# Kernel tuning notes

Hardware: AMD Instinct MI355X
Metric: run time of the kernel (lower is better)

The kernel has to match this reference:

```python
import jax, jax.numpy as jnp
import numpy as np

TEMP = 5.0          # temperature_attn
BN_EPS = 1e-5
L2_EPS = 1e-8

def _conv2d(x, w):
    # x: [N,C,H,W], w: [O,C,3,3], SAME padding, stride 1
    return jax.lax.conv_general_dilated(x, w, (1, 1), 'SAME',
                                        dimension_numbers=('NCHW', 'OIHW', 'NCHW'))

def _conv_over_base(x, w):
    # separable 4D conv piece: 2D conv over the (Hb,Wb) pair of the 6D tensor
    BN, C, Hm, Wm, Hb, Wb = x.shape
    O = w.shape[0]
    y = _conv2d(x.transpose(0, 2, 3, 1, 4, 5).reshape(BN * Hm * Wm, C, Hb, Wb), w)
    return y.reshape(BN, Hm, Wm, O, Hb, Wb).transpose(0, 3, 1, 2, 4, 5)

def _conv_over_mem(x, w):
    # separable 4D conv piece: 2D conv over the (Hm,Wm) pair of the 6D tensor
    BN, C, Hm, Wm, Hb, Wb = x.shape
    O = w.shape[0]
    y = _conv2d(x.transpose(0, 4, 5, 1, 2, 3).reshape(BN * Hb * Wb, C, Hm, Wm), w)
    return y.reshape(BN, Hb, Wb, O, Hm, Wm).transpose(0, 3, 4, 5, 1, 2)

def _l2norm(x, axis):
    n = jnp.sqrt(jnp.sum(x * x, axis=axis, keepdims=True))
    return x / jnp.maximum(n, L2_EPS)

def _gaussian_normalize(x, axis):
    m = jnp.mean(x, axis=axis, keepdims=True)
    v = jnp.var(x, axis=axis, ddof=1, keepdims=True)  # torch.var is unbiased
    return (x - m) / jnp.sqrt(v + BN_EPS)

def setup_inputs() -> dict:
    key = jax.random.key(0)
    ks = jax.random.split(key, 10)
    B, N, C, H = 8, 64, 512, 10
    R, HID, NCLS = 64, 16, 100
    f32 = jnp.float32
    return {
        'feat_b': jax.random.normal(ks[0], (B, C, H, H), f32),
        'feat_m': jax.random.normal(ks[1], (N, C, H, H), f32),
        'w1x1':  jax.random.normal(ks[2], (R, C), f32) * 0.05,     # cca_1x1 conv weight
        'bn_gamma': jnp.ones((R,), f32),
        'bn_beta':  jnp.zeros((R,), f32),
        'w1a': jax.random.normal(ks[3], (HID, 1, 3, 3), f32) * 0.3,   # CCA block1, base-pair conv
        'w1b': jax.random.normal(ks[4], (HID, HID, 3, 3), f32) * 0.1, # CCA block1, mem-pair conv
        'w2a': jax.random.normal(ks[5], (1, HID, 3, 3), f32) * 0.1,   # CCA block2, base-pair conv
        'w2b': jax.random.normal(ks[6], (1, 1, 3, 3), f32) * 0.3,     # CCA block2, mem-pair conv
        'w_fc': jax.random.normal(ks[7], (NCLS, 2 * C), f32) * 0.02,  # memory-wrap head
        'b_fc': jnp.zeros((NCLS,), f32),
    }

def reference(feat_b, feat_m, w1x1, bn_gamma, bn_beta, w1a, w1b, w2a, w2b, w_fc, b_fc):
    B, C, Hb, Wb = feat_b.shape
    N, _, Hm, Wm = feat_m.shape
    # channel mean shift
    fb_s = feat_b - feat_b.mean(axis=1, keepdims=True)
    fm_s = feat_m - feat_m.mean(axis=1, keepdims=True)
    # 1x1 conv + BatchNorm(eval: mu=0,var=1) + ReLU, then L2-normalize over channels
    def proj(x):
        y = jnp.einsum('bchw,rc->brhw', x, w1x1)
        y = jax.nn.relu(y * bn_gamma[None, :, None, None] + bn_beta[None, :, None, None])
        return _l2norm(y, axis=1)
    fbp, fmp = proj(fb_s), proj(fm_s)
    # 6D cross-correlation map [B,N,Hm,Wm,Hb,Wb]
    corr = jnp.einsum('bchw,ncij->bnijhw', fbp, fmp)
    # CCA module: two separable 4D conv blocks (1->16, ReLU, 16->1)
    x = corr.reshape(B * N, 1, Hm, Wm, Hb, Wb)
    h = jax.nn.relu(_conv_over_mem(_conv_over_base(x, w1a), w1b))
    corr = _conv_over_mem(_conv_over_base(h, w2a), w2b).reshape(B, N, Hm, Wm, Hb, Wb)
    # memory-direction normalize+softmax (over Hm*Wm)
    cm = corr.reshape(B, N, Hm * Wm, Hb, Wb)
    cm = jax.nn.softmax(_gaussian_normalize(cm, 2) / TEMP, axis=2)
    attn_memory = cm.reshape(B, N, Hm, Wm, Hb, Wb).sum(axis=(4, 5))  # [B,N,Hm,Wm]
    # batch-direction normalize+softmax (over Hb*Wb)
    cb = corr.reshape(B, N, Hm, Wm, Hb * Wb)
    cb = jax.nn.softmax(_gaussian_normalize(cb, 4) / TEMP, axis=4)
    attn_batch = cb.reshape(B, N, Hm, Wm, Hb, Wb).sum(axis=(2, 3))  # [B,N,Hb,Wb] (used only for extras)
    # per-input attended memory embedding [B,N,C]
    att_mem = jnp.einsum('bnhw,nchw->bnc', attn_memory, feat_m) / (Hm * Wm)
    # memory wrap: cosine content weights over N + linear head on [enc ; mem_vec]
    enc = feat_b.mean(axis=(2, 3))                       # [B,C]
    enc_n = _l2norm(enc, axis=1)
    mem_n = _l2norm(att_mem, axis=2)
    w = jax.nn.softmax(jnp.einsum('bc,bnc->bn', enc_n, mem_n), axis=1)
    mem_vec = jnp.einsum('bn,bnc->bc', w, att_mem)
    logits = jnp.concatenate([enc, mem_vec], axis=1) @ w_fc.T + b_fc
    return logits
```

## Files before the change

kernel.cpp:

```cpp
#include <hip/hip_runtime.h>
#include <hip/hip_bf16.h>


__global__ __launch_bounds__(512) void k_proj2(const float* __restrict__ feat_b,
                                               const float* __restrict__ feat_m,
                                               const float* __restrict__ w1x1,
                                               const float* __restrict__ gamma,
                                               const float* __restrict__ beta,
                                               float* __restrict__ fbp,
                                               float* __restrict__ fmp) {
    __shared__ __align__(16) float xt[64][104];
    __shared__ __align__(16) float wt[64][68];
    __shared__ float colsum[100];
    __shared__ float wsumL[64];
    __shared__ float invL[100];
    const int tid = threadIdx.x;
    const int img = blockIdx.x;
    const float* x;
    float* outp;
    if (img < 8) { x = feat_b + (size_t)img * 51200; outp = fbp + (size_t)img * 6400; }
    else         { x = feat_m + (size_t)(img - 8) * 51200; outp = fmp + (size_t)(img - 8) * 6400; }

    if (tid < 100) colsum[tid] = 0.f;
    if (tid < 64) wsumL[tid] = 0.f;
    const int r = tid >> 3, q = tid & 7;
    float acc[13];
#pragma unroll
    for (int j = 0; j < 13; ++j) acc[j] = 0.f;
    __syncthreads();

    for (int ct = 0; ct < 8; ++ct) {
        for (int i = tid; i < 1600; i += 512) {
            int row = i / 25, c4 = (i % 25) * 4;
            *(float4*)&xt[row][c4] = *(const float4*)&x[(size_t)(ct * 64 + row) * 100 + c4];
        }
        for (int i = tid; i < 1024; i += 512) {
            int row = i / 16, c4 = (i % 16) * 4;
            *(float4*)&wt[row][c4] = *(const float4*)&w1x1[(size_t)row * 512 + ct * 64 + c4];
        }
        __syncthreads();
        if (tid < 100) {
            float s = 0.f;
            for (int c = 0; c < 64; ++c) s += xt[c][tid];
            colsum[tid] += s;
        }
        if (tid < 64) {
            float s = 0.f;
            for (int c = 0; c < 64; ++c) s += wt[tid][c];
            wsumL[tid] += s;
        }
        for (int c = 0; c < 64; ++c) {
            float w = wt[r][c];
#pragma unroll
            for (int j = 0; j < 13; ++j) {
                int hw = q + 8 * j;
                if (hw < 100) acc[j] = fmaf(w, xt[c][hw], acc[j]);
            }
        }
        __syncthreads();
    }
    float g = gamma[r], be = beta[r], wsr = wsumL[r];
#pragma unroll
    for (int j = 0; j < 13; ++j) {
        int hw = q + 8 * j;
        if (hw < 100) {
            float mean = colsum[hw] * (1.f / 512.f);
            xt[r][hw] = fmaxf((acc[j] - mean * wsr) * g + be, 0.f);
        }
    }
    __syncthreads();
    if (tid < 100) {
        float ss = 0.f;
        for (int rr = 0; rr < 64; ++rr) { float z = xt[rr][tid]; ss = fmaf(z, z, ss); }
        invL[tid] = 1.f / fmaxf(sqrtf(ss), 1e-8f);
    }
    __syncthreads();
    for (int i = tid; i < 6400; i += 512) {
        int rr = i / 100, hw = i % 100;
        outp[i] = xt[rr][hw] * invL[hw];
    }
}

__global__ __launch_bounds__(512) void k_corr(const float* __restrict__ fbp,
                                              const float* __restrict__ fmp,
                                              const float* __restrict__ w1a,
                                              const float* __restrict__ w1b,
                                              float* __restrict__ K1c,
                                              float* __restrict__ corr) {
    if (blockIdx.x == 512) {
        for (int t = threadIdx.x; t < 1296; t += 512) {
            int dm = t / 144, rem = t % 144;
            int db = rem / 16, c = rem % 16;
            float s = 0.f;
            for (int cp = 0; cp < 16; ++cp)
                s += w1b[(c * 16 + cp) * 9 + dm] * w1a[cp * 9 + db];
            K1c[t] = s;
        }
        return;
    }
    __shared__ __align__(16) float A[6400];
    __shared__ __align__(16) float B[6400];
    const int tid = threadIdx.x, bn = blockIdx.x;
    const float* fm = fmp + (size_t)(bn & 63) * 6400;
    const float* fb = fbp + (size_t)(bn >> 6) * 6400;
    for (int i = tid * 4; i < 6400; i += 2048) {
        *(float4*)&A[i] = *(const float4*)&fm[i];
        *(float4*)&B[i] = *(const float4*)&fb[i];
    }
    __syncthreads();
    float* dst = corr + (size_t)bn * 10000;
    for (int u = tid; u < 625; u += 512) {
        int m0 = (u / 25) * 4, b0 = (u % 25) * 4;
        float acc[4][4] = {};
        for (int r = 0; r < 64; ++r) {
            float4 av = *(const float4*)&A[r * 100 + m0];
            float4 bv = *(const float4*)&B[r * 100 + b0];
            float a[4] = {av.x, av.y, av.z, av.w};
            float bb[4] = {bv.x, bv.y, bv.z, bv.w};
#pragma unroll
            for (int i = 0; i < 4; ++i)
#pragma unroll
                for (int j = 0; j < 4; ++j) acc[i][j] = fmaf(a[i], bb[j], acc[i][j]);
        }
#pragma unroll
        for (int i = 0; i < 4; ++i)
#pragma unroll
            for (int j = 0; j < 4; ++j) dst[(m0 + i) * 100 + (b0 + j)] = acc[i][j];
    }
}

__global__ __launch_bounds__(64, 4) void k_cca(const float* __restrict__ corr,
                                               const float* __restrict__ K1c,
                                               const float* __restrict__ w2a,
                                               float* __restrict__ g1out) {
    __shared__ float ring[2184];
    const int lane = threadIdx.x;
    const int wm = blockIdx.x, bn = blockIdx.y;
    const int u = lane < 50 ? lane : 49;
    const int bh = u / 5, p = u % 5, bw0 = 2 * p;
    const bool act = lane < 50;

    for (int i = lane; i < 2184; i += 64) ring[i] = 0.f;
    const float* cbase = corr + (size_t)bn * 10000 + (wm - 1) * 100;
    const int i0 = (wm == 0) ? 100 : 0;
    const int i1 = (wm == 9) ? 200 : 300;

    auto prefetch = [&](int R) {
        if (R > 9) return;
        const float* src = cbase + R * 1000;
        float* dslot = &ring[(R & 3) * 504];
#pragma unroll
        for (int k = 0; k < 5; ++k) {
            int i = lane + k * 64;
            if (i >= i0 && i < i1) {
                int mc = i / 100, t = i % 100;
                dslot[mc * 168 + (t / 10 + 1) * 14 + (t % 10 + 1)] = src[i];
            }
        }
    };
    prefetch(0);
    prefetch(1);

    const int rbase = bh * 14 + bw0;
    for (int mr = 0; mr < 10; ++mr) {
        prefetch(mr + 2);

        float a0[16], a1[16];
#pragma unroll
        for (int c = 0; c < 16; ++c) { a0[c] = 0.f; a1[c] = 0.f; }
        for (int dmh = 0; dmh < 3; ++dmh) {
            int mrow = mr + dmh - 1;
            if ((unsigned)mrow >= 10u) continue;
            const float* slab0 = &ring[(mrow & 3) * 504];
#pragma unroll
            for (int dmw = 0; dmw < 3; ++dmw) {
                bool mv = (unsigned)(wm + dmw - 1) < 10u;
                const float* cb = (mv ? slab0 + dmw * 168 : &ring[2016]) + rbase;
                const float* kp = K1c + (dmh * 3 + dmw) * 144;
#pragma unroll
                for (int dbh = 0; dbh < 3; ++dbh) {
                    float2 lo = *(const float2*)&cb[dbh * 14];
                    float2 hi = *(const float2*)&cb[dbh * 14 + 2];
                    const float* kq = kp + dbh * 48;
#pragma unroll
                    for (int c = 0; c < 16; ++c) {
                        float k0 = kq[c], k1 = kq[16 + c], k2 = kq[32 + c];
                        a0[c] = fmaf(k0, lo.x, fmaf(k1, lo.y, fmaf(k2, hi.x, a0[c])));
                        a1[c] = fmaf(k0, lo.y, fmaf(k1, hi.x, fmaf(k2, hi.y, a1[c])));
                    }
                }
            }
        }

        float P00 = 0.f, P01 = 0.f, P10 = 0.f, P11 = 0.f, P20 = 0.f, P21 = 0.f;
#pragma unroll
        for (int c = 0; c < 16; ++c) {
            float r0 = fmaxf(a0[c], 0.f), r1 = fmaxf(a1[c], 0.f);
            float lA = __shfl(r1, lane - 1); lA = (p > 0) ? lA : 0.f;
            float rA = __shfl(r0, lane + 1); rA = (p < 4) ? rA : 0.f;
            const float* wq = w2a + c * 9;
            P00 = fmaf(wq[0], lA, fmaf(wq[1], r0, fmaf(wq[2], r1, P00)));
            P01 = fmaf(wq[0], r0, fmaf(wq[1], r1, fmaf(wq[2], rA, P01)));
            P10 = fmaf(wq[3], lA, fmaf(wq[4], r0, fmaf(wq[5], r1, P10)));
            P11 = fmaf(wq[3], r0, fmaf(wq[4], r1, fmaf(wq[5], rA, P11)));
            P20 = fmaf(wq[6], lA, fmaf(wq[7], r0, fmaf(wq[8], r1, P20)));
            P21 = fmaf(wq[6], r0, fmaf(wq[7], r1, fmaf(wq[8], rA, P21)));
        }
        float u00 = __shfl(P00, lane - 5), u01 = __shfl(P01, lane - 5);
        float u20 = __shfl(P20, lane + 5), u21 = __shfl(P21, lane + 5);
        if (bh == 0) { u00 = 0.f; u01 = 0.f; }
        if (bh == 9) { u20 = 0.f; u21 = 0.f; }
        float g0 = P10 + u00 + u20;
        float g1v = P11 + u01 + u21;
        if (act) {
            float2 st; st.x = g0; st.y = g1v;
            *(float2*)&g1out[(size_t)bn * 10000 + (mr * 10 + wm) * 100 + bh * 10 + bw0] = st;
        }
    }
}

__global__ __launch_bounds__(512) void k_msoft2(const float* __restrict__ g1,
                                                const float* __restrict__ w2b,
                                                float* __restrict__ attnm) {
    __shared__ float gt[10000];
    const int tid = threadIdx.x, bn = blockIdx.x;
    const float* src = g1 + (size_t)bn * 10000;
    for (int i = tid; i < 10000; i += 512) gt[i] = src[i];
    __syncthreads();
    float wb[9];
#pragma unroll
    for (int t = 0; t < 9; ++t) wb[t] = w2b[t];
    const int b = tid >> 2, q = tid & 3;
    const bool act = tid < 400;
    float ev[25];
    float se = 0.f;
    if (act) {
        float s = 0.f, ss = 0.f;
#pragma unroll
        for (int i = 0; i < 25; ++i) {
            int m = q * 25 + i, mh = m / 10, mw = m % 10;
            float v = 0.f;
#pragma unroll
            for (int dh = 0; dh < 3; ++dh) {
                int rr = mh + dh - 1;
                if ((unsigned)rr < 10u) {
#pragma unroll
                    for (int dw = 0; dw < 3; ++dw) {
                        int ww = mw + dw - 1;
                        if ((unsigned)ww < 10u)
                            v = fmaf(wb[dh * 3 + dw], gt[(rr * 10 + ww) * 100 + b], v);
                    }
                }
            }
            ev[i] = v;
            s += v; ss = fmaf(v, v, ss);
        }
        s += __shfl_xor(s, 1); s += __shfl_xor(s, 2);
        ss += __shfl_xor(ss, 1); ss += __shfl_xor(ss, 2);
        float mean = s * 0.01f;
        float var = (ss - 100.f * mean * mean) * (1.f / 99.f);
        float istd = 0.2f / sqrtf(var + 1e-5f);
        float mx = -1e30f;
#pragma unroll
        for (int i = 0; i < 25; ++i) mx = fmaxf(mx, ev[i]);
        mx = fmaxf(mx, __shfl_xor(mx, 1)); mx = fmaxf(mx, __shfl_xor(mx, 2));
#pragma unroll
        for (int i = 0; i < 25; ++i) {
            float e = expf((ev[i] - mx) * istd);
            ev[i] = e; se += e;
        }
        se += __shfl_xor(se, 1); se += __shfl_xor(se, 2);
    }
    __syncthreads();
    if (act) {
        float inv = 1.f / se;
#pragma unroll
        for (int i = 0; i < 25; ++i) gt[(q * 25 + i) * 100 + b] = ev[i] * inv;
    }
    __syncthreads();
    if (act) {
        int m = tid >> 2;
        float s2 = 0.f;
#pragma unroll
        for (int i = 0; i < 25; ++i) s2 += gt[m * 100 + q * 25 + i];
        s2 += __shfl_xor(s2, 1); s2 += __shfl_xor(s2, 2);
        if (q == 0) attnm[bn * 100 + m] = s2;
    }
}

__global__ __launch_bounds__(128) void k_attmem(const float* __restrict__ attnm,
                                                const float* __restrict__ feat_m,
                                                float* __restrict__ attm) {
    __shared__ float A[8][100];
    int n = blockIdx.x, cq = blockIdx.y, tid = threadIdx.x;
    for (int i = tid; i < 800; i += 128) {
        int b = i / 100, m = i % 100;
        A[b][m] = attnm[(b * 64 + n) * 100 + m];
    }
    __syncthreads();
    int c = cq * 128 + tid;
    const float* fp = feat_m + ((size_t)n * 512 + c) * 100;
    float acc[8] = {};
    for (int m4 = 0; m4 < 100; m4 += 4) {
        float4 v = *(const float4*)&fp[m4];
#pragma unroll
        for (int b = 0; b < 8; ++b) {
            acc[b] = fmaf(A[b][m4], v.x, acc[b]);
            acc[b] = fmaf(A[b][m4 + 1], v.y, acc[b]);
            acc[b] = fmaf(A[b][m4 + 2], v.z, acc[b]);
            acc[b] = fmaf(A[b][m4 + 3], v.w, acc[b]);
        }
    }
#pragma unroll
    for (int b = 0; b < 8; ++b)
        attm[((size_t)(b * 64 + n)) * 512 + c] = acc[b] * 0.01f;
}

__global__ __launch_bounds__(512) void k_final(const float* __restrict__ feat_b,
                                               const float* __restrict__ attm,
                                               const float* __restrict__ w_fc,
                                               const float* __restrict__ b_fc,
                                               float* __restrict__ out) {
    __shared__ float attL[64 * 513];
    __shared__ float encL[512];
    __shared__ float mv[512];
    __shared__ float wL[64];
    __shared__ float red[512];
    int b = blockIdx.x, tid = threadIdx.x;
    {
        const float* fp = feat_b + ((size_t)b * 512 + tid) * 100;
        float s = 0.f;
        for (int m = 0; m < 100; m += 4) {
            float4 v = *(const float4*)&fp[m];
            s += v.x + v.y + v.z + v.w;
        }
        float e = s * 0.01f;
        encL[tid] = e;
        red[tid] = e * e;
    }
    const float* ap = attm + (size_t)b * 32768;
    for (int i = tid; i < 32768; i += 512) attL[(i >> 9) * 513 + (i & 511)] = ap[i];
    __syncthreads();
    for (int o = 256; o; o >>= 1) {
        if (tid < o) red[tid] += red[tid + o];
        __syncthreads();
    }
    float escale = 1.f / fmaxf(sqrtf(red[0]), 1e-8f);
    if (tid < 64) {
        int n = tid;
        float ss = 0.f, dp = 0.f;
        for (int c = 0; c < 512; ++c) {
            float a = attL[n * 513 + c];
            ss = fmaf(a, a, ss);
            dp = fmaf(encL[c], a, dp);
        }
        float sc = dp * escale / fmaxf(sqrtf(ss), 1e-8f);
        float mx = sc;
#pragma unroll
        for (int o = 32; o; o >>= 1) mx = fmaxf(mx, __shfl_xor(mx, o));
        float e = expf(sc - mx);
        float seL = e;
#pragma unroll
        for (int o = 32; o; o >>= 1) seL += __shfl_xor(seL, o);
        wL[n] = e / seL;
    }
    __syncthreads();
    {
        int c = tid;
        float s = 0.f;
        for (int n = 0; n < 64; ++n) s = fmaf(wL[n], attL[n * 513 + c], s);
        mv[c] = s;
    }
    __syncthreads();
    for (int k = tid; k < 100; k += 512) {
        const float* wp = w_fc + (size_t)k * 1024;
        float acc = b_fc[k];
        for (int c = 0; c < 512; c += 4) {
            float4 w0 = *(const float4*)&wp[c];
            float4 w1 = *(const float4*)&wp[512 + c];
            acc = fmaf(encL[c], w0.x, acc);     acc = fmaf(encL[c + 1], w0.y, acc);
            acc = fmaf(encL[c + 2], w0.z, acc); acc = fmaf(encL[c + 3], w0.w, acc);
            acc = fmaf(mv[c], w1.x, acc);       acc = fmaf(mv[c + 1], w1.y, acc);
            acc = fmaf(mv[c + 2], w1.z, acc);   acc = fmaf(mv[c + 3], w1.w, acc);
        }
        out[b * 100 + k] = acc;
    }
}

extern "C" void kernel_launch(void* const* d_in, const int* in_sizes, int n_in,
                              void* d_out, int out_size, void* d_ws, size_t ws_size,
                              hipStream_t stream) {
    const float* feat_b = (const float*)d_in[0];
    const float* feat_m = (const float*)d_in[1];
    const float* w1x1   = (const float*)d_in[2];
    const float* gamma  = (const float*)d_in[3];
    const float* beta   = (const float*)d_in[4];
    const float* w1a    = (const float*)d_in[5];
    const float* w1b    = (const float*)d_in[6];
    const float* w2a    = (const float*)d_in[7];
    const float* w2b    = (const float*)d_in[8];
    const float* w_fc   = (const float*)d_in[9];
    const float* b_fc   = (const float*)d_in[10];

    float* ws    = (float*)d_ws;
    float* K1c   = ws;
    float* fbp   = ws + 1312;
    float* fmp   = fbp + 51200;
    float* corr  = fmp + 409600;
    float* g1    = corr + 5120000;
    float* attnm = g1 + 5120000;
    float* attm  = attnm + 51200;

    hipLaunchKernelGGL(k_proj2, dim3(72), dim3(512), 0, stream,
                       feat_b, feat_m, w1x1, gamma, beta, fbp, fmp);
    hipLaunchKernelGGL(k_corr, dim3(513), dim3(512), 0, stream,
                       fbp, fmp, w1a, w1b, K1c, corr);
    hipLaunchKernelGGL(k_cca, dim3(10, 512), dim3(64), 0, stream,
                       corr, K1c, w2a, g1);
    hipLaunchKernelGGL(k_msoft2, dim3(512), dim3(512), 0, stream, g1, w2b, attnm);
    hipLaunchKernelGGL(k_attmem, dim3(64, 4), dim3(128), 0, stream, attnm, feat_m, attm);
    hipLaunchKernelGGL(k_final, dim3(8), dim3(512), 0, stream,
                       feat_b, attm, w_fc, b_fc, (float*)d_out);
}
```

Measured before the change: 349.8 us.

## Use Winograd F(2,3) transform in CCA conv and split rows across grid z

Precomputes Winograd-transformed combined kernels (four per tap and channel) so each pair of output columns in the first CCA convolution needs four multiplies per channel instead of six. It also splits the 10 memory rows into two halves across a new grid dimension, doubling block count and shortening the per-block serial loop. In exchange the halo rows are prefetched redundantly by both halves, the transformed kernel takes more workspace, and the rounding changes slightly.

```diff
diff --git a/kernel.cpp b/kernel.cpp
--- a/kernel.cpp
+++ b/kernel.cpp
@@ -85,16 +85,24 @@
                                               const float* __restrict__ fmp,
                                               const float* __restrict__ w1a,
                                               const float* __restrict__ w1b,
-                                              float* __restrict__ K1c,
+                                              float* __restrict__ K1w,
                                               float* __restrict__ corr) {
     if (blockIdx.x == 512) {
-        for (int t = threadIdx.x; t < 1296; t += 512) {
-            int dm = t / 144, rem = t % 144;
-            int db = rem / 16, c = rem % 16;
-            float s = 0.f;
-            for (int cp = 0; cp < 16; ++cp)
-                s += w1b[(c * 16 + cp) * 9 + dm] * w1a[cp * 9 + db];
-            K1c[t] = s;
+        for (int t = threadIdx.x; t < 432; t += 512) {
+            int tap = t >> 4, c = t & 15;
+            int dm = tap / 3, dbh = tap % 3;
+            float g0 = 0.f, g1 = 0.f, g2 = 0.f;
+            for (int cp = 0; cp < 16; ++cp) {
+                float wb = w1b[(c * 16 + cp) * 9 + dm];
+                g0 = fmaf(wb, w1a[cp * 9 + dbh * 3 + 0], g0);
+                g1 = fmaf(wb, w1a[cp * 9 + dbh * 3 + 1], g1);
+                g2 = fmaf(wb, w1a[cp * 9 + dbh * 3 + 2], g2);
+            }
+            int base = tap * 64 + c;
+            K1w[base]      = g0;
+            K1w[base + 16] = 0.5f * (g0 + g1 + g2);
+            K1w[base + 32] = 0.5f * (g0 - g1 + g2);
+            K1w[base + 48] = g2;
         }
         return;
     }
@@ -130,12 +138,14 @@
 }
 
 __global__ __launch_bounds__(64, 4) void k_cca(const float* __restrict__ corr,
-                                               const float* __restrict__ K1c,
+                                               const float* __restrict__ K1w,
                                                const float* __restrict__ w2a,
                                                float* __restrict__ g1out) {
     __shared__ float ring[2184];
     const int lane = threadIdx.x;
     const int wm = blockIdx.x, bn = blockIdx.y;
+    const int mr_lo = blockIdx.z * 5, mr_hi = mr_lo + 4;
+    const int R_max = (mr_hi + 1 < 9) ? mr_hi + 1 : 9;
     const int u = lane < 50 ? lane : 49;
     const int bh = u / 5, p = u % 5, bw0 = 2 * p;
     const bool act = lane < 50;
@@ -146,7 +156,7 @@
     const int i1 = (wm == 9) ? 200 : 300;
 
     auto prefetch = [&](int R) {
-        if (R > 9) return;
+        if (R < 0 || R > R_max) return;
         const float* src = cbase + R * 1000;
         float* dslot = &ring[(R & 3) * 504];
 #pragma unroll
@@ -158,16 +168,17 @@
             }
         }
     };
-    prefetch(0);
-    prefetch(1);
+    prefetch(mr_lo - 1);
+    prefetch(mr_lo);
+    prefetch(mr_lo + 1);
 
     const int rbase = bh * 14 + bw0;
-    for (int mr = 0; mr < 10; ++mr) {
+    for (int mr = mr_lo; mr <= mr_hi; ++mr) {
         prefetch(mr + 2);
 
-        float a0[16], a1[16];
-#pragma unroll
-        for (int c = 0; c < 16; ++c) { a0[c] = 0.f; a1[c] = 0.f; }
+        float A1[16], A2[16], A3[16], A4[16];
+#pragma unroll
+        for (int c = 0; c < 16; ++c) { A1[c] = 0.f; A2[c] = 0.f; A3[c] = 0.f; A4[c] = 0.f; }
         for (int dmh = 0; dmh < 3; ++dmh) {
             int mrow = mr + dmh - 1;
             if ((unsigned)mrow >= 10u) continue;
@@ -176,17 +187,22 @@
             for (int dmw = 0; dmw < 3; ++dmw) {
                 bool mv = (unsigned)(wm + dmw - 1) < 10u;
                 const float* cb = (mv ? slab0 + dmw * 168 : &ring[2016]) + rbase;
-                const float* kp = K1c + (dmh * 3 + dmw) * 144;
+                const float* kp = K1w + (dmh * 3 + dmw) * 192;
 #pragma unroll
                 for (int dbh = 0; dbh < 3; ++dbh) {
                     float2 lo = *(const float2*)&cb[dbh * 14];
                     float2 hi = *(const float2*)&cb[dbh * 14 + 2];
-                    const float* kq = kp + dbh * 48;
+                    float t1 = lo.x - hi.x;
+                    float t2 = lo.y + hi.x;
+                    float t3 = hi.x - lo.y;
+                    float t4 = lo.y - hi.y;
+                    const float* kq = kp + dbh * 64;
 #pragma unroll
                     for (int c = 0; c < 16; ++c) {
-                        float k0 = kq[c], k1 = kq[16 + c], k2 = kq[32 + c];
-                        a0[c] = fmaf(k0, lo.x, fmaf(k1, lo.y, fmaf(k2, hi.x, a0[c])));
-                        a1[c] = fmaf(k0, lo.y, fmaf(k1, hi.x, fmaf(k2, hi.y, a1[c])));
+                        A1[c] = fmaf(t1, kq[c], A1[c]);
+                        A2[c] = fmaf(t2, kq[16 + c], A2[c]);
+                        A3[c] = fmaf(t3, kq[32 + c], A3[c]);
+                        A4[c] = fmaf(t4, kq[48 + c], A4[c]);
                     }
                 }
             }
@@ -195,7 +211,8 @@
         float P00 = 0.f, P01 = 0.f, P10 = 0.f, P11 = 0.f, P20 = 0.f, P21 = 0.f;
 #pragma unroll
         for (int c = 0; c < 16; ++c) {
-            float r0 = fmaxf(a0[c], 0.f), r1 = fmaxf(a1[c], 0.f);
+            float r0 = fmaxf(A1[c] + A2[c] + A3[c], 0.f);
+            float r1 = fmaxf(A2[c] - A3[c] - A4[c], 0.f);
             float lA = __shfl(r1, lane - 1); lA = (p > 0) ? lA : 0.f;
             float rA = __shfl(r0, lane + 1); rA = (p < 4) ? rA : 0.f;
             const float* wq = w2a + c * 9;
@@ -403,8 +420,8 @@
     const float* b_fc   = (const float*)d_in[10];
 
     float* ws    = (float*)d_ws;
-    float* K1c   = ws;
-    float* fbp   = ws + 1312;
+    float* K1w   = ws;
+    float* fbp   = ws + 1760;
     float* fmp   = fbp + 51200;
     float* corr  = fmp + 409600;
     float* g1    = corr + 5120000;
@@ -414,9 +431,9 @@
     hipLaunchKernelGGL(k_proj2, dim3(72), dim3(512), 0, stream,
                        feat_b, feat_m, w1x1, gamma, beta, fbp, fmp);
     hipLaunchKernelGGL(k_corr, dim3(513), dim3(512), 0, stream,
-                       fbp, fmp, w1a, w1b, K1c, corr);
-    hipLaunchKernelGGL(k_cca, dim3(10, 512), dim3(64), 0, stream,
-                       corr, K1c, w2a, g1);
+                       fbp, fmp, w1a, w1b, K1w, corr);
+    hipLaunchKernelGGL(k_cca, dim3(10, 512, 2), dim3(64), 0, stream,
+                       corr, K1w, w2a, g1);
     hipLaunchKernelGGL(k_msoft2, dim3(512), dim3(512), 0, stream, g1, w2b, attnm);
     hipLaunchKernelGGL(k_attmem, dim3(64, 4), dim3(128), 0, stream, attnm, feat_m, attm);
     hipLaunchKernelGGL(k_final, dim3(8), dim3(512), 0, stream,
```

After: 323.2 us. -7.6%, faster.
